# Kernel optimization log

Measured on AMD Instinct MI355X. Metric: run time of the kernel, lower is better.

Reference implementation:

```python
import jax, jax.numpy as jnp
import numpy as np

B, S, E = 2, 2048, 1024
H = 16
HD = E // H  # 64


def setup_inputs() -> dict:
    key = jax.random.key(0)
    ks = jax.random.split(key, 9)
    sc = 1.0 / np.sqrt(E)
    return {
        "X": jax.random.normal(ks[0], (B, S, E), jnp.float32),
        "Wq": jax.random.normal(ks[1], (E, E), jnp.float32) * sc,
        "bq": jax.random.normal(ks[2], (E,), jnp.float32) * sc,
        "Wk": jax.random.normal(ks[3], (E, E), jnp.float32) * sc,
        "bk": jax.random.normal(ks[4], (E,), jnp.float32) * sc,
        "Wv": jax.random.normal(ks[5], (E, E), jnp.float32) * sc,
        "bv": jax.random.normal(ks[6], (E,), jnp.float32) * sc,
        "Wo": jax.random.normal(ks[7], (E, E), jnp.float32) * sc,
        "bo": jax.random.normal(ks[8], (E,), jnp.float32) * sc,
    }


def reference(X, Wq, bq, Wk, bk, Wv, bv, Wo, bo):
    b, s, e = X.shape
    # torch Linear: x @ W.T + b (weights stored (out, in))
    Q = X @ Wq.T + bq
    K = X @ Wk.T + bk
    V = X @ Wv.T + bv
    # (b, s, E) -> (b, H, s, HD)
    Q = Q.reshape(b, s, H, HD).transpose(0, 2, 1, 3)
    K = K.reshape(b, s, H, HD).transpose(0, 2, 1, 3)
    V = V.reshape(b, s, H, HD).transpose(0, 2, 1, 3)
    scores = jnp.einsum("bhqd,bhkd->bhqk", Q, K) / np.sqrt(HD).astype(np.float32)
    attn = jax.nn.softmax(scores, axis=-1)
    ctx = jnp.einsum("bhqk,bhkd->bhqd", attn, V)  # (b, H, s, HD)
    # Faithful to original: reshape (b,H,s,HD) -> (b,s,E) WITHOUT permuting heads back
    ctx = ctx.reshape(b, s, e)
    return ctx @ Wo.T + bo
```

## Files before the change

### kernel.cpp

```cpp
#include <hip/hip_runtime.h>


typedef __bf16 bf16x8 __attribute__((ext_vector_type(8)));
typedef __bf16 bf16x4 __attribute__((ext_vector_type(4)));
typedef float f32x4 __attribute__((ext_vector_type(4)));
typedef unsigned short ushort_t;

#define S_LEN 2048
#define E_DIM 1024
#define H_NUM 16
#define HD_DIM 64

__device__ __forceinline__ ushort_t f2bf(float f) {
  union { float f; unsigned u; } v; v.f = f;
  unsigned u = v.u;
  unsigned r = (u + 0x7FFFu + ((u >> 16) & 1u)) >> 16;
  return (ushort_t)r;
}

#define GLDS16(gp, lp)                                              \
  __builtin_amdgcn_global_load_lds(                                 \
      (const __attribute__((address_space(1))) unsigned int*)(gp),  \
      (__attribute__((address_space(3))) unsigned int*)(lp), 16, 0, 0)

__global__ __launch_bounds__(256) void cvt_all(
    const float* __restrict__ X, const float* __restrict__ Wq,
    const float* __restrict__ Wk, const float* __restrict__ Wv,
    const float* __restrict__ Wo, ushort_t* __restrict__ Xbf,
    ushort_t* __restrict__ Wqkv, ushort_t* __restrict__ Wob) {
  int i = blockIdx.x * 256 + threadIdx.x;
  const float* src;
  ushort_t* dst;
  int off;
  if (i < 1048576) {
    src = X; dst = Xbf; off = i;
  } else if (i < 1310720) {
    src = Wq; dst = Wqkv; off = i - 1048576;
  } else if (i < 1572864) {
    src = Wk; dst = Wqkv + (1 << 20); off = i - 1310720;
  } else if (i < 1835008) {
    src = Wv; dst = Wqkv + (2 << 20); off = i - 1572864;
  } else {
    src = Wo; dst = Wob; off = i - 1835008;
  }
  float4 v = ((const float4*)src)[off];
  ushort4 o;
  o.x = f2bf(v.x); o.y = f2bf(v.y); o.z = f2bf(v.z); o.w = f2bf(v.w);
  ((ushort4*)dst)[off] = o;
}

__global__ __launch_bounds__(256) void gemm_qkv(
    const ushort_t* __restrict__ Xbf, const ushort_t* __restrict__ Wqkv,
    const float* __restrict__ bq, const float* __restrict__ bk,
    const float* __restrict__ bv,
    ushort_t* __restrict__ Qb, ushort_t* __restrict__ Kb,
    ushort_t* __restrict__ Vb) {
  __shared__ ushort_t As[128 * 64];
  __shared__ ushort_t Bs[128 * 64];
  const int t = threadIdx.x;
  const int w = t >> 6, lane = t & 63, quad = lane >> 4, lr = lane & 15;
  const int m0 = blockIdx.y * 128, n0 = blockIdx.x * 128;
  const int wm = (w & 1) * 64, wn = (w >> 1) * 64;
  const int matid = n0 >> 10;
  const int nl0 = n0 & 1023;

  const int srow = t >> 3;
  const int gsrc = (t & 7) ^ (srow & 7);
  const ushort_t* Ag = Xbf + (size_t)(m0 + srow) * E_DIM + gsrc * 8;
  const ushort_t* Bg = Wqkv + (size_t)matid * E_DIM * E_DIM +
                       (size_t)(nl0 + srow) * E_DIM + gsrc * 8;

  f32x4 acc[4][4] = {};

  for (int kt = 0; kt < E_DIM / 64; ++kt) {
#pragma unroll
    for (int r = 0; r < 4; r++) {
      GLDS16(Ag + (size_t)r * 32 * E_DIM, As + r * 2048 + t * 8);
      GLDS16(Bg + (size_t)r * 32 * E_DIM, Bs + r * 2048 + t * 8);
    }
    Ag += 64; Bg += 64;
    __syncthreads();
#pragma unroll
    for (int kk = 0; kk < 2; kk++) {
      bf16x8 af[4], bfr[4];
      const int gs0 = (kk * 4 + quad) ^ (lr & 7);
#pragma unroll
      for (int i = 0; i < 4; i++) {
        af[i]  = *(const bf16x8*)(As + (wm + i * 16 + lr) * 64 + gs0 * 8);
        bfr[i] = *(const bf16x8*)(Bs + (wn + i * 16 + lr) * 64 + gs0 * 8);
      }
#pragma unroll
      for (int i = 0; i < 4; i++)
#pragma unroll
        for (int j = 0; j < 4; j++)
          acc[i][j] = __builtin_amdgcn_mfma_f32_16x16x32_bf16(
              af[i], bfr[j], acc[i][j], 0, 0, 0);
    }
    __syncthreads();
  }

  const float* bias_p = (matid == 0) ? bq : (matid == 1) ? bk : bv;
  ushort_t* dst = (matid == 0) ? Qb : (matid == 1) ? Kb : Vb;
  const float scl = (matid == 0) ? 0.125f : 1.0f;
#pragma unroll
  for (int j = 0; j < 4; j++) {
    int col = n0 + wn + j * 16 + lr;
    int cl = col & 1023;
    int h = cl >> 6, d = cl & 63;
    float bias = bias_p[cl];
#pragma unroll
    for (int i = 0; i < 4; i++) {
#pragma unroll
      for (int r = 0; r < 4; r++) {
        int row = m0 + wm + i * 16 + quad * 4 + r;
        int bb = row >> 11, ss = row & 2047;
        size_t o = ((size_t)((bb * H_NUM + h) * S_LEN + ss)) * HD_DIM + d;
        dst[o] = f2bf((acc[i][j][r] + bias) * scl);
      }
    }
  }
}

__global__ __launch_bounds__(256) void vtrans(
    const ushort_t* __restrict__ Vb, ushort_t* __restrict__ Vt) {
  __shared__ ushort_t tile[64 * 72];
  const int bh = blockIdx.y;
  const int s0 = blockIdx.x * 64;
  const int t = threadIdx.x;
  {
    const int sr = t >> 2, c0 = (t & 3) * 16;
    const ushort_t* src = Vb + ((size_t)bh * S_LEN + s0 + sr) * HD_DIM + c0;
    *(uint4*)(&tile[sr * 72 + c0]) = *(const uint4*)(src);
    *(uint4*)(&tile[sr * 72 + c0 + 8]) = *(const uint4*)(src + 8);
  }
  __syncthreads();
  const int d = t >> 2, c = t & 3;
  ushort_t v[16];
#pragma unroll
  for (int w = 0; w < 16; w++) {
    int key = (w & 3) * 16 + 4 * c + (w >> 2);
    v[w] = tile[key * 72 + d];
  }
  ushort_t* dst = Vt + ((size_t)bh * HD_DIM + d) * S_LEN + s0 + 16 * c;
  *(uint4*)(dst) = *(const uint4*)(v);
  *(uint4*)(dst + 8) = *(const uint4*)(v + 8);
}

__global__ __launch_bounds__(256) void attn(
    const ushort_t* __restrict__ Qb, const ushort_t* __restrict__ Kb,
    const ushort_t* __restrict__ Vt, ushort_t* __restrict__ Ctx) {
  __shared__ ushort_t KV[2 * 64 * 64];
  __shared__ ushort_t Ps[64 * 72];
  ushort_t* Ks = KV;
  ushort_t* Vs = KV + 4096;
  const int t = threadIdx.x, w = t >> 6, lane = t & 63;
  const int quad = lane >> 4, lr = lane & 15;
  const int bh = blockIdx.y, q0 = blockIdx.x * 64;
  const ushort_t* Qg = Qb + ((size_t)bh * S_LEN + q0) * HD_DIM;
  const ushort_t* Kg = Kb + (size_t)bh * S_LEN * HD_DIM;
  const ushort_t* Vg = Vt + (size_t)bh * HD_DIM * S_LEN;

  const int srow = t >> 3;
  const int gsrc = (t & 7) ^ (srow & 7);

#pragma unroll
  for (int r = 0; r < 2; r++)
    GLDS16(Qg + (size_t)(r * 32 + srow) * HD_DIM + gsrc * 8,
           KV + r * 2048 + t * 8);
  __syncthreads();
  bf16x8 qf[2];
#pragma unroll
  for (int kc = 0; kc < 2; kc++) {
    int row = w * 16 + lr;
    int gs = (kc * 4 + quad) ^ (lr & 7);
    qf[kc] = *(const bf16x8*)(KV + row * 64 + gs * 8);
  }

  f32x4 cacc[4] = {};
  float psum[4] = {};

  for (int kt = 0; kt < S_LEN / 64; ++kt) {
    const int k0 = kt * 64;
    __syncthreads();
#pragma unroll
    for (int r = 0; r < 2; r++) {
      GLDS16(Kg + (size_t)(k0 + r * 32 + srow) * HD_DIM + gsrc * 8,
             Ks + r * 2048 + t * 8);
      GLDS16(Vg + (size_t)(r * 32 + srow) * S_LEN + k0 + gsrc * 8,
             Vs + r * 2048 + t * 8);
    }
    __syncthreads();

    f32x4 sacc[4] = {};
#pragma unroll
    for (int nt = 0; nt < 4; nt++) {
#pragma unroll
      for (int kc = 0; kc < 2; kc++) {
        int gs = (kc * 4 + quad) ^ (lr & 7);
        bf16x8 kf = *(const bf16x8*)(Ks + (nt * 16 + lr) * 64 + gs * 8);
        sacc[nt] = __builtin_amdgcn_mfma_f32_16x16x32_bf16(
            qf[kc], kf, sacc[nt], 0, 0, 0);
      }
    }

#pragma unroll
    for (int i = 0; i < 4; i++) {
      float p0 = __expf(sacc[0][i]);
      float p1 = __expf(sacc[1][i]);
      float p2 = __expf(sacc[2][i]);
      float p3 = __expf(sacc[3][i]);
      psum[i] += (p0 + p1) + (p2 + p3);
      bf16x4 pv;
      pv[0] = (__bf16)p0; pv[1] = (__bf16)p1;
      pv[2] = (__bf16)p2; pv[3] = (__bf16)p3;
      int row = w * 16 + quad * 4 + i;
      *(bf16x4*)(Ps + row * 72 + lr * 4) = pv;
    }

#pragma unroll
    for (int kc = 0; kc < 2; kc++) {
      bf16x8 pf =
          *(const bf16x8*)(Ps + (w * 16 + lr) * 72 + kc * 32 + quad * 8);
#pragma unroll
      for (int dt = 0; dt < 4; dt++) {
        int gs = (kc * 4 + quad) ^ (lr & 7);
        bf16x8 vf = *(const bf16x8*)(Vs + (dt * 16 + lr) * 64 + gs * 8);
        cacc[dt] = __builtin_amdgcn_mfma_f32_16x16x32_bf16(
            pf, vf, cacc[dt], 0, 0, 0);
      }
    }
  }

#pragma unroll
  for (int i = 0; i < 4; i++) {
    float rs = psum[i];
    rs += __shfl_xor(rs, 1);
    rs += __shfl_xor(rs, 2);
    rs += __shfl_xor(rs, 4);
    rs += __shfl_xor(rs, 8);
    float inv = 1.0f / rs;
    int srow2 = q0 + w * 16 + quad * 4 + i;
#pragma unroll
    for (int dt = 0; dt < 4; dt++)
      Ctx[((size_t)bh * S_LEN + srow2) * HD_DIM + dt * 16 + lr] =
          f2bf(cacc[dt][i] * inv);
  }
}

__global__ __launch_bounds__(256) void gemm_out(
    const ushort_t* __restrict__ Cb, const ushort_t* __restrict__ Wob,
    const float* __restrict__ bo, float* __restrict__ out) {
  __shared__ ushort_t As[128 * 64];
  __shared__ ushort_t Bs[128 * 64];
  const int t = threadIdx.x;
  const int w = t >> 6, lane = t & 63, quad = lane >> 4, lr = lane & 15;
  const int m0 = blockIdx.y * 128, n0 = blockIdx.x * 128;
  const int wm = (w & 1) * 64, wn = (w >> 1) * 64;

  const int srow = t >> 3;
  const int gsrc = (t & 7) ^ (srow & 7);
  const ushort_t* Ag = Cb + (size_t)(m0 + srow) * E_DIM + gsrc * 8;
  const ushort_t* Bg = Wob + (size_t)(n0 + srow) * E_DIM + gsrc * 8;

  f32x4 acc[4][4] = {};

  for (int kt = 0; kt < E_DIM / 64; ++kt) {
#pragma unroll
    for (int r = 0; r < 4; r++) {
      GLDS16(Ag + (size_t)r * 32 * E_DIM, As + r * 2048 + t * 8);
      GLDS16(Bg + (size_t)r * 32 * E_DIM, Bs + r * 2048 + t * 8);
    }
    Ag += 64; Bg += 64;
    __syncthreads();
#pragma unroll
    for (int kk = 0; kk < 2; kk++) {
      bf16x8 af[4], bfr[4];
      const int gs0 = (kk * 4 + quad) ^ (lr & 7);
#pragma unroll
      for (int i = 0; i < 4; i++) {
        af[i]  = *(const bf16x8*)(As + (wm + i * 16 + lr) * 64 + gs0 * 8);
        bfr[i] = *(const bf16x8*)(Bs + (wn + i * 16 + lr) * 64 + gs0 * 8);
      }
#pragma unroll
      for (int i = 0; i < 4; i++)
#pragma unroll
        for (int j = 0; j < 4; j++)
          acc[i][j] = __builtin_amdgcn_mfma_f32_16x16x32_bf16(
              af[i], bfr[j], acc[i][j], 0, 0, 0);
    }
    __syncthreads();
  }

#pragma unroll
  for (int j = 0; j < 4; j++) {
    int col = n0 + wn + j * 16 + lr;
    float bias = bo[col];
#pragma unroll
    for (int i = 0; i < 4; i++) {
#pragma unroll
      for (int r = 0; r < 4; r++) {
        int row = m0 + wm + i * 16 + quad * 4 + r;
        out[(size_t)row * E_DIM + col] = acc[i][j][r] + bias;
      }
    }
  }
}

extern "C" void kernel_launch(void* const* d_in, const int* in_sizes, int n_in,
                              void* d_out, int out_size, void* d_ws,
                              size_t ws_size, hipStream_t stream) {
  const float* X  = (const float*)d_in[0];
  const float* bq = (const float*)d_in[2];
  const float* bk = (const float*)d_in[4];
  const float* bv = (const float*)d_in[6];
  const float* Wo = (const float*)d_in[7];
  const float* bo = (const float*)d_in[8];
  float* out = (float*)d_out;

  char* ws = (char*)d_ws;
  ushort_t* Xbf  = (ushort_t*)(ws);
  ushort_t* Wqkv = (ushort_t*)(ws + ((size_t)8 << 20));
  ushort_t* Wob  = (ushort_t*)(ws + ((size_t)14 << 20));
  ushort_t* Qb   = (ushort_t*)(ws + ((size_t)16 << 20));
  ushort_t* Kb   = (ushort_t*)(ws + ((size_t)24 << 20));
  ushort_t* Vb   = (ushort_t*)(ws + ((size_t)32 << 20));
  ushort_t* Vt   = (ushort_t*)(ws + ((size_t)40 << 20));
  ushort_t* Cb   = (ushort_t*)(ws + ((size_t)48 << 20));

  cvt_all<<<8192, 256, 0, stream>>>(X, (const float*)d_in[1],
                                    (const float*)d_in[3],
                                    (const float*)d_in[5], Wo, Xbf, Wqkv, Wob);

  gemm_qkv<<<dim3(24, 32), 256, 0, stream>>>(Xbf, Wqkv, bq, bk, bv, Qb, Kb, Vb);
  vtrans<<<dim3(32, 32), 256, 0, stream>>>(Vb, Vt);
  attn<<<dim3(32, 32), 256, 0, stream>>>(Qb, Kb, Vt, Cb);
  gemm_out<<<dim3(8, 32), 256, 0, stream>>>(Cb, Wob, bo, out);
}
```

Measured before the change: 212.1 us.

## Fuse V transpose into QKV GEMM, double-buffer attention K/V, shrink output GEMM tiles

The QKV GEMM epilogue now writes V directly in the permuted transposed layout the attention kernel expects, which removes the separate vtrans kernel and its extra round trip through memory. The attention kernel double-buffers K/V tiles in shared memory, prefetching the next tile while computing the current one, and drops one barrier per iteration. The output GEMM switches from 128x128 to 64x64 tiles, quadrupling the grid to fill more CUs. In exchange, the V epilogue does scattered stores and attention needs twice the K/V LDS footprint.

Measured after the change: 213.7 us. About the same (+0.8%).

```diff
diff --git a/kernel.cpp b/kernel.cpp
--- a/kernel.cpp
+++ b/kernel.cpp
@@ -54,7 +54,7 @@
     const float* __restrict__ bq, const float* __restrict__ bk,
     const float* __restrict__ bv,
     ushort_t* __restrict__ Qb, ushort_t* __restrict__ Kb,
-    ushort_t* __restrict__ Vb) {
+    ushort_t* __restrict__ Vt) {
   __shared__ ushort_t As[128 * 64];
   __shared__ ushort_t Bs[128 * 64];
   const int t = threadIdx.x;
@@ -100,59 +100,51 @@
   }
 
   const float* bias_p = (matid == 0) ? bq : (matid == 1) ? bk : bv;
-  ushort_t* dst = (matid == 0) ? Qb : (matid == 1) ? Kb : Vb;
-  const float scl = (matid == 0) ? 0.125f : 1.0f;
-#pragma unroll
-  for (int j = 0; j < 4; j++) {
-    int col = n0 + wn + j * 16 + lr;
-    int cl = col & 1023;
-    int h = cl >> 6, d = cl & 63;
-    float bias = bias_p[cl];
-#pragma unroll
-    for (int i = 0; i < 4; i++) {
-#pragma unroll
-      for (int r = 0; r < 4; r++) {
-        int row = m0 + wm + i * 16 + quad * 4 + r;
-        int bb = row >> 11, ss = row & 2047;
-        size_t o = ((size_t)((bb * H_NUM + h) * S_LEN + ss)) * HD_DIM + d;
-        dst[o] = f2bf((acc[i][j][r] + bias) * scl);
-      }
-    }
-  }
-}
-
-__global__ __launch_bounds__(256) void vtrans(
-    const ushort_t* __restrict__ Vb, ushort_t* __restrict__ Vt) {
-  __shared__ ushort_t tile[64 * 72];
-  const int bh = blockIdx.y;
-  const int s0 = blockIdx.x * 64;
-  const int t = threadIdx.x;
-  {
-    const int sr = t >> 2, c0 = (t & 3) * 16;
-    const ushort_t* src = Vb + ((size_t)bh * S_LEN + s0 + sr) * HD_DIM + c0;
-    *(uint4*)(&tile[sr * 72 + c0]) = *(const uint4*)(src);
-    *(uint4*)(&tile[sr * 72 + c0 + 8]) = *(const uint4*)(src + 8);
-  }
-  __syncthreads();
-  const int d = t >> 2, c = t & 3;
-  ushort_t v[16];
-#pragma unroll
-  for (int w = 0; w < 16; w++) {
-    int key = (w & 3) * 16 + 4 * c + (w >> 2);
-    v[w] = tile[key * 72 + d];
-  }
-  ushort_t* dst = Vt + ((size_t)bh * HD_DIM + d) * S_LEN + s0 + 16 * c;
-  *(uint4*)(dst) = *(const uint4*)(v);
-  *(uint4*)(dst + 8) = *(const uint4*)(v + 8);
+  if (matid < 2) {
+    ushort_t* dst = (matid == 0) ? Qb : Kb;
+    const float scl = (matid == 0) ? 0.125f : 1.0f;
+#pragma unroll
+    for (int j = 0; j < 4; j++) {
+      int cl = (n0 + wn + j * 16 + lr) & 1023;
+      int h = cl >> 6, d = cl & 63;
+      float bias = bias_p[cl];
+#pragma unroll
+      for (int i = 0; i < 4; i++) {
+#pragma unroll
+        for (int r = 0; r < 4; r++) {
+          int row = m0 + wm + i * 16 + quad * 4 + r;
+          int bb = row >> 11, ss = row & 2047;
+          size_t o = ((size_t)((bb * H_NUM + h) * S_LEN + ss)) * HD_DIM + d;
+          dst[o] = f2bf((acc[i][j][r] + bias) * scl);
+        }
+      }
+    }
+  } else {
+#pragma unroll
+    for (int j = 0; j < 4; j++) {
+      int cl = (n0 + wn + j * 16 + lr) & 1023;
+      int h = cl >> 6, d = cl & 63;
+      float bias = bias_p[cl];
+#pragma unroll
+      for (int i = 0; i < 4; i++) {
+#pragma unroll
+        for (int r = 0; r < 4; r++) {
+          int row = m0 + wm + i * 16 + quad * 4 + r;
+          int bb = row >> 11, ss = row & 2047;
+          size_t o = ((size_t)((bb * H_NUM + h) * HD_DIM + d)) * S_LEN +
+                     (ss & ~63) + ((ss & 15) * 4) + ((ss >> 4) & 3);
+          Vt[o] = f2bf(acc[i][j][r] + bias);
+        }
+      }
+    }
+  }
 }
 
 __global__ __launch_bounds__(256) void attn(
     const ushort_t* __restrict__ Qb, const ushort_t* __restrict__ Kb,
     const ushort_t* __restrict__ Vt, ushort_t* __restrict__ Ctx) {
-  __shared__ ushort_t KV[2 * 64 * 64];
+  __shared__ ushort_t KV[2 * 8192];
   __shared__ ushort_t Ps[64 * 72];
-  ushort_t* Ks = KV;
-  ushort_t* Vs = KV + 4096;
   const int t = threadIdx.x, w = t >> 6, lane = t & 63;
   const int quad = lane >> 4, lr = lane & 15;
   const int bh = blockIdx.y, q0 = blockIdx.x * 64;
@@ -164,32 +156,41 @@
   const int gsrc = (t & 7) ^ (srow & 7);
 
 #pragma unroll
-  for (int r = 0; r < 2; r++)
+  for (int r = 0; r < 2; r++) {
     GLDS16(Qg + (size_t)(r * 32 + srow) * HD_DIM + gsrc * 8,
+           Ps + r * 2048 + t * 8);
+    GLDS16(Kg + (size_t)(r * 32 + srow) * HD_DIM + gsrc * 8,
            KV + r * 2048 + t * 8);
+    GLDS16(Vg + (size_t)(r * 32 + srow) * S_LEN + gsrc * 8,
+           KV + 4096 + r * 2048 + t * 8);
+  }
   __syncthreads();
   bf16x8 qf[2];
 #pragma unroll
   for (int kc = 0; kc < 2; kc++) {
-    int row = w * 16 + lr;
     int gs = (kc * 4 + quad) ^ (lr & 7);
-    qf[kc] = *(const bf16x8*)(KV + row * 64 + gs * 8);
-  }
+    qf[kc] = *(const bf16x8*)(Ps + (w * 16 + lr) * 64 + gs * 8);
+  }
+  __syncthreads();
+
+  const ushort_t* kp = Kg + srow * HD_DIM + gsrc * 8 + 64 * HD_DIM;
+  const ushort_t* vp = Vg + srow * S_LEN + gsrc * 8 + 64;
 
   f32x4 cacc[4] = {};
   float psum[4] = {};
 
   for (int kt = 0; kt < S_LEN / 64; ++kt) {
-    const int k0 = kt * 64;
-    __syncthreads();
-#pragma unroll
-    for (int r = 0; r < 2; r++) {
-      GLDS16(Kg + (size_t)(k0 + r * 32 + srow) * HD_DIM + gsrc * 8,
-             Ks + r * 2048 + t * 8);
-      GLDS16(Vg + (size_t)(r * 32 + srow) * S_LEN + k0 + gsrc * 8,
-             Vs + r * 2048 + t * 8);
-    }
-    __syncthreads();
+    const ushort_t* Kbuf = KV + (kt & 1) * 8192;
+    const ushort_t* Vbuf = Kbuf + 4096;
+    if (kt + 1 < S_LEN / 64) {
+      ushort_t* nb = KV + ((kt + 1) & 1) * 8192;
+      GLDS16(kp, nb + t * 8);
+      GLDS16(kp + 32 * HD_DIM, nb + 2048 + t * 8);
+      GLDS16(vp, nb + 4096 + t * 8);
+      GLDS16(vp + 32 * S_LEN, nb + 6144 + t * 8);
+      kp += 64 * HD_DIM;
+      vp += 64;
+    }
 
     f32x4 sacc[4] = {};
 #pragma unroll
@@ -197,7 +198,7 @@
 #pragma unroll
       for (int kc = 0; kc < 2; kc++) {
         int gs = (kc * 4 + quad) ^ (lr & 7);
-        bf16x8 kf = *(const bf16x8*)(Ks + (nt * 16 + lr) * 64 + gs * 8);
+        bf16x8 kf = *(const bf16x8*)(Kbuf + (nt * 16 + lr) * 64 + gs * 8);
         sacc[nt] = __builtin_amdgcn_mfma_f32_16x16x32_bf16(
             qf[kc], kf, sacc[nt], 0, 0, 0);
       }
@@ -224,11 +225,12 @@
 #pragma unroll
       for (int dt = 0; dt < 4; dt++) {
         int gs = (kc * 4 + quad) ^ (lr & 7);
-        bf16x8 vf = *(const bf16x8*)(Vs + (dt * 16 + lr) * 64 + gs * 8);
+        bf16x8 vf = *(const bf16x8*)(Vbuf + (dt * 16 + lr) * 64 + gs * 8);
         cacc[dt] = __builtin_amdgcn_mfma_f32_16x16x32_bf16(
             pf, vf, cacc[dt], 0, 0, 0);
       }
     }
+    __syncthreads();
   }
 
 #pragma unroll
@@ -250,23 +252,23 @@
 __global__ __launch_bounds__(256) void gemm_out(
     const ushort_t* __restrict__ Cb, const ushort_t* __restrict__ Wob,
     const float* __restrict__ bo, float* __restrict__ out) {
-  __shared__ ushort_t As[128 * 64];
-  __shared__ ushort_t Bs[128 * 64];
+  __shared__ ushort_t As[64 * 64];
+  __shared__ ushort_t Bs[64 * 64];
   const int t = threadIdx.x;
   const int w = t >> 6, lane = t & 63, quad = lane >> 4, lr = lane & 15;
-  const int m0 = blockIdx.y * 128, n0 = blockIdx.x * 128;
-  const int wm = (w & 1) * 64, wn = (w >> 1) * 64;
+  const int m0 = blockIdx.y * 64, n0 = blockIdx.x * 64;
+  const int wm = (w & 1) * 32, wn = (w >> 1) * 32;
 
   const int srow = t >> 3;
   const int gsrc = (t & 7) ^ (srow & 7);
   const ushort_t* Ag = Cb + (size_t)(m0 + srow) * E_DIM + gsrc * 8;
   const ushort_t* Bg = Wob + (size_t)(n0 + srow) * E_DIM + gsrc * 8;
 
-  f32x4 acc[4][4] = {};
+  f32x4 acc[2][2] = {};
 
   for (int kt = 0; kt < E_DIM / 64; ++kt) {
 #pragma unroll
-    for (int r = 0; r < 4; r++) {
+    for (int r = 0; r < 2; r++) {
       GLDS16(Ag + (size_t)r * 32 * E_DIM, As + r * 2048 + t * 8);
       GLDS16(Bg + (size_t)r * 32 * E_DIM, Bs + r * 2048 + t * 8);
     }
@@ -274,17 +276,17 @@
     __syncthreads();
 #pragma unroll
     for (int kk = 0; kk < 2; kk++) {
-      bf16x8 af[4], bfr[4];
+      bf16x8 af[2], bfr[2];
       const int gs0 = (kk * 4 + quad) ^ (lr & 7);
 #pragma unroll
-      for (int i = 0; i < 4; i++) {
+      for (int i = 0; i < 2; i++) {
         af[i]  = *(const bf16x8*)(As + (wm + i * 16 + lr) * 64 + gs0 * 8);
         bfr[i] = *(const bf16x8*)(Bs + (wn + i * 16 + lr) * 64 + gs0 * 8);
       }
 #pragma unroll
-      for (int i = 0; i < 4; i++)
-#pragma unroll
-        for (int j = 0; j < 4; j++)
+      for (int i = 0; i < 2; i++)
+#pragma unroll
+        for (int j = 0; j < 2; j++)
           acc[i][j] = __builtin_amdgcn_mfma_f32_16x16x32_bf16(
               af[i], bfr[j], acc[i][j], 0, 0, 0);
     }
@@ -292,11 +294,11 @@
   }
 
 #pragma unroll
-  for (int j = 0; j < 4; j++) {
+  for (int j = 0; j < 2; j++) {
     int col = n0 + wn + j * 16 + lr;
     float bias = bo[col];
 #pragma unroll
-    for (int i = 0; i < 4; i++) {
+    for (int i = 0; i < 2; i++) {
 #pragma unroll
       for (int r = 0; r < 4; r++) {
         int row = m0 + wm + i * 16 + quad * 4 + r;
@@ -323,16 +325,14 @@
   ushort_t* Wob  = (ushort_t*)(ws + ((size_t)14 << 20));
   ushort_t* Qb   = (ushort_t*)(ws + ((size_t)16 << 20));
   ushort_t* Kb   = (ushort_t*)(ws + ((size_t)24 << 20));
-  ushort_t* Vb   = (ushort_t*)(ws + ((size_t)32 << 20));
-  ushort_t* Vt   = (ushort_t*)(ws + ((size_t)40 << 20));
-  ushort_t* Cb   = (ushort_t*)(ws + ((size_t)48 << 20));
+  ushort_t* Vt   = (ushort_t*)(ws + ((size_t)32 << 20));
+  ushort_t* Cb   = (ushort_t*)(ws + ((size_t)40 << 20));
 
   cvt_all<<<8192, 256, 0, stream>>>(X, (const float*)d_in[1],
                                     (const float*)d_in[3],
                                     (const float*)d_in[5], Wo, Xbf, Wqkv, Wob);
 
-  gemm_qkv<<<dim3(24, 32), 256, 0, stream>>>(Xbf, Wqkv, bq, bk, bv, Qb, Kb, Vb);
-  vtrans<<<dim3(32, 32), 256, 0, stream>>>(Vb, Vt);
+  gemm_qkv<<<dim3(24, 32), 256, 0, stream>>>(Xbf, Wqkv, bq, bk, bv, Qb, Kb, Vt);
   attn<<<dim3(32, 32), 256, 0, stream>>>(Qb, Kb, Vt, Cb);
-  gemm_out<<<dim3(8, 32), 256, 0, stream>>>(Cb, Wob, bo, out);
-}
+  gemm_out<<<dim3(16, 64), 256, 0, stream>>>(Cb, Wob, bo, out);
+}
```
